# Optimization experiments

Measured on AMD Instinct MI355X. Metric: run time of the kernel, lower is better.

Reference implementation:

```python
import jax, jax.numpy as jnp
import numpy as np

B, L, F, R = 8, 64, 64, 2048

def setup_inputs() -> dict:
    key = jax.random.key(0)
    k1, k2, k3, k4, k5, k6, k7 = jax.random.split(key, 7)
    return {
        "x": jax.random.normal(k1, (B, L, F, R), dtype=jnp.float32),
        "arg1_weight": jax.random.uniform(k2, (B, L), dtype=jnp.float32),
        "arg2_weight": jax.random.uniform(k3, (B, L), dtype=jnp.float32),
        "root_filler": jax.random.normal(k4, (B, F), dtype=jnp.float32),
        "cons_l": jax.random.normal(k5, (R, R), dtype=jnp.float32) / np.sqrt(R).astype(np.float32),
        "cons_r": jax.random.normal(k6, (R, R), dtype=jnp.float32) / np.sqrt(R).astype(np.float32),
        "root_role": jax.random.normal(k7, (R,), dtype=jnp.float32),
    }

def reference(x, arg1_weight, arg2_weight, root_filler, cons_l, cons_r, root_role):
    # Weighted reduction over memory slots: [B,L,F,R] x [B,L] -> [B,F,R]
    arg1 = jnp.einsum('blfr,bl->bfr', x, arg1_weight)
    arg2 = jnp.einsum('blfr,bl->bfr', x, arg2_weight)
    # F.linear on last (role) dim: y = arg @ W^T, plus root outer product
    output = (jnp.einsum('bfr,sr->bfs', arg1, cons_l)
              + jnp.einsum('bfr,sr->bfs', arg2, cons_r)
              + root_filler[:, :, None] * root_role[None, None, :])
    max1 = jnp.max(arg1_weight, axis=1)
    max2 = jnp.max(arg2_weight, axis=1)
    return (output, max1, max2)
```

## Files before the change

kernel.cpp:

```cpp
#include <hip/hip_runtime.h>
#include <hip/hip_bf16.h>
#include <stdint.h>

#define B_DIM 8
#define L_DIM 64
#define F_DIM 64
#define R_DIM 2048
#define M_DIM 512
#define K_DIM 4096
#define N_DIM 2048

typedef _Float16 half_t;
typedef _Float16 half4 __attribute__((ext_vector_type(4)));
typedef _Float16 half8 __attribute__((ext_vector_type(8)));
typedef float floatx4 __attribute__((ext_vector_type(4)));
typedef float f4 __attribute__((ext_vector_type(4)));

__global__ __launch_bounds__(512) void k_front(
    const float* __restrict__ x, const float* __restrict__ w1,
    const float* __restrict__ w2, const float* __restrict__ cl,
    const float* __restrict__ cr, half_t* __restrict__ Ah,
    half_t* __restrict__ Bh, float* __restrict__ out)
{
    const int tid = threadIdx.x;
    const int bid = blockIdx.x;

    if (bid < 512) {
        __shared__ float w1s[L_DIM], w2s[L_DIM];
        const int bf = bid;
        const int b  = bf >> 6;
        const int f  = bf & 63;
        if (tid < L_DIM) {
            w1s[tid] = w1[b * L_DIM + tid];
            w2s[tid] = w2[b * L_DIM + tid];
        }
        __syncthreads();
        const int r0 = tid * 4;
        const f4* xp = (const f4*)(x + ((size_t)(b * 4096 + f)) * 2048 + r0);
        float a1x=0.f,a1y=0.f,a1z=0.f,a1w=0.f;
        float a2x=0.f,a2y=0.f,a2z=0.f,a2w=0.f;
        #pragma unroll 8
        for (int l = 0; l < L_DIM; ++l) {
            f4 v = __builtin_nontemporal_load(xp + (size_t)l * (F_DIM * R_DIM / 4));
            float u1 = w1s[l], u2 = w2s[l];
            a1x += v.x*u1; a1y += v.y*u1; a1z += v.z*u1; a1w += v.w*u1;
            a2x += v.x*u2; a2y += v.y*u2; a2z += v.z*u2; a2w += v.w*u2;
        }
        half4 h1 = { (half_t)a1x, (half_t)a1y, (half_t)a1z, (half_t)a1w };
        half4 h2 = { (half_t)a2x, (half_t)a2y, (half_t)a2z, (half_t)a2w };
        *(half4*)(Ah + (size_t)bf * K_DIM + r0) = h1;
        *(half4*)(Ah + (size_t)bf * K_DIM + R_DIM + r0) = h2;
    } else if (bid < 2560) {
        const int i = ((bid - 512) * 512 + tid) * 4;
        const int s = i >> 11;
        const int r = i & 2047;
        f4 vl = __builtin_nontemporal_load((const f4*)(cl + i));
        f4 vr = __builtin_nontemporal_load((const f4*)(cr + i));
        half4 hl = { (half_t)vl.x, (half_t)vl.y, (half_t)vl.z, (half_t)vl.w };
        half4 hr = { (half_t)vr.x, (half_t)vr.y, (half_t)vr.z, (half_t)vr.w };
        *(half4*)(Bh + (size_t)s * K_DIM + r) = hl;
        *(half4*)(Bh + (size_t)s * K_DIM + R_DIM + r) = hr;
    } else {
        if (tid < 16) {
            const float* src = (tid < 8) ? w1 : w2;
            const int b = tid & 7;
            float m = -1.f;
            #pragma unroll 8
            for (int l = 0; l < L_DIM; ++l)
                m = fmaxf(m, src[b * L_DIM + l]);
            out[M_DIM * N_DIM + tid] = m;
        }
    }
}

__device__ __forceinline__ void gload16(void* lds, const void* g)
{
    __builtin_amdgcn_global_load_lds(
        (const __attribute__((address_space(1))) void*)g,
        (__attribute__((address_space(3))) void*)lds, 16, 0, 0);
}

#define BM 128
#define BN 128
#define BK 64
#define SPLITK 8
#define KSEG (K_DIM / SPLITK)
#define NSTEP (KSEG / BK)

__global__ __launch_bounds__(256) void k_gemm(
    const half_t* __restrict__ Ah, const half_t* __restrict__ Bh,
    float* __restrict__ part)
{
    __shared__ half_t sA[2][BM * BK];
    __shared__ half_t sB[2][BN * BK];
    const int tid  = threadIdx.x;
    const int lane = tid & 63;
    const int w    = tid >> 6;
    const int wr   = w >> 1, wc = w & 1;
    const int m0   = blockIdx.y * BM;
    const int n0   = blockIdx.x * BN;
    const int kz   = blockIdx.z * KSEG;

    const int srow = lane >> 3;
    const int scol = ((lane & 7) ^ srow) << 3;

    const floatx4 fzero = { 0.f, 0.f, 0.f, 0.f };
    floatx4 acc[4][4];
    #pragma unroll
    for (int i = 0; i < 4; ++i)
        #pragma unroll
        for (int j = 0; j < 4; ++j) acc[i][j] = fzero;

    auto stage = [&](int buf, int kt) {
        #pragma unroll
        for (int c = 0; c < 4; ++c) {
            const int rbase = w * 32 + c * 8;
            const int row   = rbase + srow;
            gload16(&sA[buf][rbase * BK], Ah + (size_t)(m0 + row) * K_DIM + kt + scol);
            gload16(&sB[buf][rbase * BK], Bh + (size_t)(n0 + row) * K_DIM + kt + scol);
        }
    };

    stage(0, kz);
    __syncthreads();

    const int l15 = lane & 15, l4 = lane >> 4;
    int buf = 0;
    for (int ks = 0; ks < NSTEP; ++ks) {
        if (ks + 1 < NSTEP) stage(buf ^ 1, kz + (ks + 1) * BK);
        #pragma unroll
        for (int ksub = 0; ksub < 2; ++ksub) {
            half8 af[4], bfr[4];
            const int cb = ksub * 4 + l4;
            #pragma unroll
            for (int mi = 0; mi < 4; ++mi) {
                const int row = wr * 64 + mi * 16 + l15;
                af[mi] = *(const half8*)&sA[buf][row * BK + ((cb ^ (row & 7)) << 3)];
            }
            #pragma unroll
            for (int ni = 0; ni < 4; ++ni) {
                const int row = wc * 64 + ni * 16 + l15;
                bfr[ni] = *(const half8*)&sB[buf][row * BK + ((cb ^ (row & 7)) << 3)];
            }
            #pragma unroll
            for (int mi = 0; mi < 4; ++mi)
                #pragma unroll
                for (int ni = 0; ni < 4; ++ni)
                    acc[mi][ni] = __builtin_amdgcn_mfma_f32_16x16x32_f16(
                        af[mi], bfr[ni], acc[mi][ni], 0, 0, 0);
        }
        __syncthreads();
        buf ^= 1;
    }

    float* P = part + (size_t)blockIdx.z * ((size_t)M_DIM * N_DIM);
    #pragma unroll
    for (int mi = 0; mi < 4; ++mi) {
        const int rb = m0 + wr * 64 + mi * 16 + l4 * 4;
        #pragma unroll
        for (int ni = 0; ni < 4; ++ni) {
            const int cc = n0 + wc * 64 + ni * 16 + l15;
            #pragma unroll
            for (int r = 0; r < 4; ++r)
                P[(size_t)(rb + r) * N_DIM + cc] = acc[mi][ni][r];
        }
    }
}

__global__ __launch_bounds__(256) void k_final(
    const float* __restrict__ part, const float* __restrict__ filler,
    const float* __restrict__ role, float* __restrict__ out)
{
    const int idx = (blockIdx.x * 256 + threadIdx.x) * 4;
    const int mfi = idx >> 11;
    const int s   = idx & 2047;
    float4 a = *(const float4*)(part + idx);
    #pragma unroll
    for (int z = 1; z < SPLITK; ++z) {
        float4 p = *(const float4*)(part + (size_t)z * (M_DIM * N_DIM) + idx);
        a.x += p.x; a.y += p.y; a.z += p.z; a.w += p.w;
    }
    const float fl = filler[mfi];
    float4 ro = *(const float4*)(role + s);
    a.x += fl * ro.x; a.y += fl * ro.y; a.z += fl * ro.z; a.w += fl * ro.w;
    *(float4*)(out + idx) = a;
}

extern "C" void kernel_launch(void* const* d_in, const int* in_sizes, int n_in,
                              void* d_out, int out_size, void* d_ws, size_t ws_size,
                              hipStream_t stream)
{
    const float* x      = (const float*)d_in[0];
    const float* w1     = (const float*)d_in[1];
    const float* w2     = (const float*)d_in[2];
    const float* filler = (const float*)d_in[3];
    const float* cl     = (const float*)d_in[4];
    const float* cr     = (const float*)d_in[5];
    const float* role   = (const float*)d_in[6];
    float* out = (float*)d_out;

    char* ws = (char*)d_ws;
    half_t* Ah  = (half_t*)ws;
    half_t* Bh  = (half_t*)(ws + (4u << 20));
    float*  prt = (float*)(ws + (20u << 20));

    hipLaunchKernelGGL(k_front, dim3(2561), dim3(512), 0, stream,
                       x, w1, w2, cl, cr, Ah, Bh, out);
    hipLaunchKernelGGL(k_gemm,  dim3(N_DIM / BN, M_DIM / BM, SPLITK), dim3(256), 0, stream,
                       Ah, Bh, prt);
    hipLaunchKernelGGL(k_final, dim3(1024), dim3(256), 0, stream, prt, filler, role, out);
}
```

Before: 82.22 us.

## Fuse front, GEMM and reduction into one cooperative persistent kernel

Replaces the three launches (reduce/convert, split-K GEMM, final sum) with a single cooperative kernel of 256 blocks separated by grid-wide syncs. Split-K drops from 8 to 4 and the per-block GEMM tile becomes 128x128 across 8 waves, each computing 64x32. The aim is to remove launch gaps and shrink the partial-sum traffic. The cost is far fewer blocks and waves in the memory-bound front phase (256 blocks instead of 2561), plus grid-sync overhead.

Measured after the change: 298.3 us. +262.8%, slower.

```diff
diff --git a/kernel.cpp b/kernel.cpp
--- a/kernel.cpp
+++ b/kernel.cpp
@@ -1,77 +1,24 @@
 #include <hip/hip_runtime.h>
-#include <hip/hip_bf16.h>
+#include <hip/hip_cooperative_groups.h>
 #include <stdint.h>
 
-#define B_DIM 8
+namespace cg = cooperative_groups;
+
 #define L_DIM 64
-#define F_DIM 64
 #define R_DIM 2048
 #define M_DIM 512
 #define K_DIM 4096
 #define N_DIM 2048
+#define SPLITK 4
+#define KSEG (K_DIM / SPLITK)
+#define BK 64
+#define NSTEP (KSEG / BK)
 
 typedef _Float16 half_t;
 typedef _Float16 half4 __attribute__((ext_vector_type(4)));
 typedef _Float16 half8 __attribute__((ext_vector_type(8)));
+typedef float f4 __attribute__((ext_vector_type(4)));
 typedef float floatx4 __attribute__((ext_vector_type(4)));
-typedef float f4 __attribute__((ext_vector_type(4)));
-
-__global__ __launch_bounds__(512) void k_front(
-    const float* __restrict__ x, const float* __restrict__ w1,
-    const float* __restrict__ w2, const float* __restrict__ cl,
-    const float* __restrict__ cr, half_t* __restrict__ Ah,
-    half_t* __restrict__ Bh, float* __restrict__ out)
-{
-    const int tid = threadIdx.x;
-    const int bid = blockIdx.x;
-
-    if (bid < 512) {
-        __shared__ float w1s[L_DIM], w2s[L_DIM];
-        const int bf = bid;
-        const int b  = bf >> 6;
-        const int f  = bf & 63;
-        if (tid < L_DIM) {
-            w1s[tid] = w1[b * L_DIM + tid];
-            w2s[tid] = w2[b * L_DIM + tid];
-        }
-        __syncthreads();
-        const int r0 = tid * 4;
-        const f4* xp = (const f4*)(x + ((size_t)(b * 4096 + f)) * 2048 + r0);
-        float a1x=0.f,a1y=0.f,a1z=0.f,a1w=0.f;
-        float a2x=0.f,a2y=0.f,a2z=0.f,a2w=0.f;
-        #pragma unroll 8
-        for (int l = 0; l < L_DIM; ++l) {
-            f4 v = __builtin_nontemporal_load(xp + (size_t)l * (F_DIM * R_DIM / 4));
-            float u1 = w1s[l], u2 = w2s[l];
-            a1x += v.x*u1; a1y += v.y*u1; a1z += v.z*u1; a1w += v.w*u1;
-            a2x += v.x*u2; a2y += v.y*u2; a2z += v.z*u2; a2w += v.w*u2;
-        }
-        half4 h1 = { (half_t)a1x, (half_t)a1y, (half_t)a1z, (half_t)a1w };
-        half4 h2 = { (half_t)a2x, (half_t)a2y, (half_t)a2z, (half_t)a2w };
-        *(half4*)(Ah + (size_t)bf * K_DIM + r0) = h1;
-        *(half4*)(Ah + (size_t)bf * K_DIM + R_DIM + r0) = h2;
-    } else if (bid < 2560) {
-        const int i = ((bid - 512) * 512 + tid) * 4;
-        const int s = i >> 11;
-        const int r = i & 2047;
-        f4 vl = __builtin_nontemporal_load((const f4*)(cl + i));
-        f4 vr = __builtin_nontemporal_load((const f4*)(cr + i));
-        half4 hl = { (half_t)vl.x, (half_t)vl.y, (half_t)vl.z, (half_t)vl.w };
-        half4 hr = { (half_t)vr.x, (half_t)vr.y, (half_t)vr.z, (half_t)vr.w };
-        *(half4*)(Bh + (size_t)s * K_DIM + r) = hl;
-        *(half4*)(Bh + (size_t)s * K_DIM + R_DIM + r) = hr;
-    } else {
-        if (tid < 16) {
-            const float* src = (tid < 8) ? w1 : w2;
-            const int b = tid & 7;
-            float m = -1.f;
-            #pragma unroll 8
-            for (int l = 0; l < L_DIM; ++l)
-                m = fmaxf(m, src[b * L_DIM + l]);
-            out[M_DIM * N_DIM + tid] = m;
-        }
-    }
-}
 
 __device__ __forceinline__ void gload16(void* lds, const void* g)
 {
@@ -80,110 +27,178 @@
         (__attribute__((address_space(3))) void*)lds, 16, 0, 0);
 }
 
-#define BM 128
-#define BN 128
-#define BK 64
-#define SPLITK 8
-#define KSEG (K_DIM / SPLITK)
-#define NSTEP (KSEG / BK)
-
-__global__ __launch_bounds__(256) void k_gemm(
-    const half_t* __restrict__ Ah, const half_t* __restrict__ Bh,
-    float* __restrict__ part)
+__global__ __launch_bounds__(512, 2) void k_all(
+    const float* __restrict__ x, const float* __restrict__ w1,
+    const float* __restrict__ w2, const float* __restrict__ cl,
+    const float* __restrict__ cr, const float* __restrict__ filler,
+    const float* __restrict__ role, half_t* __restrict__ Ah,
+    half_t* __restrict__ Bh, float* __restrict__ part,
+    float* __restrict__ out)
 {
-    __shared__ half_t sA[2][BM * BK];
-    __shared__ half_t sB[2][BN * BK];
-    const int tid  = threadIdx.x;
-    const int lane = tid & 63;
-    const int w    = tid >> 6;
-    const int wr   = w >> 1, wc = w & 1;
-    const int m0   = blockIdx.y * BM;
-    const int n0   = blockIdx.x * BN;
-    const int kz   = blockIdx.z * KSEG;
-
-    const int srow = lane >> 3;
-    const int scol = ((lane & 7) ^ srow) << 3;
-
-    const floatx4 fzero = { 0.f, 0.f, 0.f, 0.f };
-    floatx4 acc[4][4];
+    __shared__ char smem[65536];
+    const int tid = threadIdx.x;
+    const int bid = blockIdx.x;
+    cg::grid_group grid = cg::this_grid();
+
+    {
+        float* w1s = (float*)smem;
+        float* w2s = w1s + L_DIM;
+        const int b = bid >> 5;
+        if (tid < L_DIM) {
+            w1s[tid] = w1[b * L_DIM + tid];
+            w2s[tid] = w2[b * L_DIM + tid];
+        }
+        __syncthreads();
+
+        #pragma unroll
+        for (int rr = 0; rr < 2; ++rr) {
+            const int bf = bid * 2 + rr;
+            const int f  = bf & 63;
+            const int r0 = tid * 4;
+            const f4* xp = (const f4*)(x + ((size_t)(b * 4096 + f)) * 2048 + r0);
+            float a1x=0.f,a1y=0.f,a1z=0.f,a1w=0.f;
+            float a2x=0.f,a2y=0.f,a2z=0.f,a2w=0.f;
+            #pragma unroll 8
+            for (int l = 0; l < L_DIM; ++l) {
+                f4 v = __builtin_nontemporal_load(xp + (size_t)l * (64 * R_DIM / 4));
+                float u1 = w1s[l], u2 = w2s[l];
+                a1x += v.x*u1; a1y += v.y*u1; a1z += v.z*u1; a1w += v.w*u1;
+                a2x += v.x*u2; a2y += v.y*u2; a2z += v.z*u2; a2w += v.w*u2;
+            }
+            half4 h1 = { (half_t)a1x, (half_t)a1y, (half_t)a1z, (half_t)a1w };
+            half4 h2 = { (half_t)a2x, (half_t)a2y, (half_t)a2z, (half_t)a2w };
+            *(half4*)(Ah + (size_t)bf * K_DIM + r0) = h1;
+            *(half4*)(Ah + (size_t)bf * K_DIM + R_DIM + r0) = h2;
+        }
+
+        #pragma unroll
+        for (int it = 0; it < 8; ++it) {
+            const int i = ((it * 131072) + bid * 512 + tid) * 4;
+            const int s = i >> 11;
+            const int r = i & 2047;
+            f4 vl = __builtin_nontemporal_load((const f4*)(cl + i));
+            f4 vr = __builtin_nontemporal_load((const f4*)(cr + i));
+            half4 hl = { (half_t)vl.x, (half_t)vl.y, (half_t)vl.z, (half_t)vl.w };
+            half4 hr = { (half_t)vr.x, (half_t)vr.y, (half_t)vr.z, (half_t)vr.w };
+            *(half4*)(Bh + (size_t)s * K_DIM + r) = hl;
+            *(half4*)(Bh + (size_t)s * K_DIM + R_DIM + r) = hr;
+        }
+
+        if (bid == 0 && tid < 16) {
+            const float* src = (tid < 8) ? w1 : w2;
+            const int b8 = tid & 7;
+            float m = -1.f;
+            #pragma unroll 8
+            for (int l = 0; l < L_DIM; ++l)
+                m = fmaxf(m, src[b8 * L_DIM + l]);
+            out[(size_t)M_DIM * N_DIM + tid] = m;
+        }
+    }
+
+    __threadfence();
+    grid.sync();
+
+    {
+        const int lane = tid & 63;
+        const int w    = tid >> 6;
+        const int wr   = w >> 2;
+        const int wc   = w & 3;
+        const int z    = bid >> 6;
+        const int mblk = (bid >> 4) & 3;
+        const int nblk = bid & 15;
+        const int m0   = mblk * 128;
+        const int n0   = nblk * 128;
+        const int kz   = z * KSEG;
+
+        const int srow = lane >> 3;
+        const int scol = ((lane & 7) ^ srow) << 3;
+
+        const floatx4 fzero = { 0.f, 0.f, 0.f, 0.f };
+        floatx4 acc[4][2];
+        #pragma unroll
+        for (int i = 0; i < 4; ++i)
+            #pragma unroll
+            for (int j = 0; j < 2; ++j) acc[i][j] = fzero;
+
+        auto stage = [&](int buf, int kt) {
+            half_t* sA = (half_t*)smem + buf * 8192;
+            half_t* sB = (half_t*)(smem + 32768) + buf * 8192;
+            #pragma unroll
+            for (int c = 0; c < 2; ++c) {
+                const int rbase = w * 16 + c * 8;
+                const int row   = rbase + srow;
+                gload16(&sA[rbase * 64], Ah + (size_t)(m0 + row) * K_DIM + kt + scol);
+                gload16(&sB[rbase * 64], Bh + (size_t)(n0 + row) * K_DIM + kt + scol);
+            }
+        };
+
+        stage(0, kz);
+        __syncthreads();
+
+        const int l15 = lane & 15, l4 = lane >> 4;
+        int buf = 0;
+        for (int ks = 0; ks < NSTEP; ++ks) {
+            if (ks + 1 < NSTEP) stage(buf ^ 1, kz + (ks + 1) * BK);
+            half_t* sA = (half_t*)smem + buf * 8192;
+            half_t* sB = (half_t*)(smem + 32768) + buf * 8192;
+            #pragma unroll
+            for (int ksub = 0; ksub < 2; ++ksub) {
+                half8 af[4], bf2[2];
+                const int cb = ksub * 4 + l4;
+                #pragma unroll
+                for (int mi = 0; mi < 4; ++mi) {
+                    const int row = wr * 64 + mi * 16 + l15;
+                    af[mi] = *(const half8*)&sA[row * 64 + ((cb ^ (row & 7)) << 3)];
+                }
+                #pragma unroll
+                for (int ni = 0; ni < 2; ++ni) {
+                    const int row = wc * 32 + ni * 16 + l15;
+                    bf2[ni] = *(const half8*)&sB[row * 64 + ((cb ^ (row & 7)) << 3)];
+                }
+                #pragma unroll
+                for (int mi = 0; mi < 4; ++mi)
+                    #pragma unroll
+                    for (int ni = 0; ni < 2; ++ni)
+                        acc[mi][ni] = __builtin_amdgcn_mfma_f32_16x16x32_f16(
+                            af[mi], bf2[ni], acc[mi][ni], 0, 0, 0);
+            }
+            __syncthreads();
+            buf ^= 1;
+        }
+
+        float* P = part + (size_t)z * ((size_t)M_DIM * N_DIM);
+        #pragma unroll
+        for (int mi = 0; mi < 4; ++mi) {
+            const int rb = m0 + wr * 64 + mi * 16 + l4 * 4;
+            #pragma unroll
+            for (int ni = 0; ni < 2; ++ni) {
+                const int cc = n0 + wc * 32 + ni * 16 + l15;
+                #pragma unroll
+                for (int r = 0; r < 4; ++r)
+                    P[(size_t)(rb + r) * N_DIM + cc] = acc[mi][ni][r];
+            }
+        }
+    }
+
+    __threadfence();
+    grid.sync();
+
     #pragma unroll
-    for (int i = 0; i < 4; ++i)
-        #pragma unroll
-        for (int j = 0; j < 4; ++j) acc[i][j] = fzero;
-
-    auto stage = [&](int buf, int kt) {
-        #pragma unroll
-        for (int c = 0; c < 4; ++c) {
-            const int rbase = w * 32 + c * 8;
-            const int row   = rbase + srow;
-            gload16(&sA[buf][rbase * BK], Ah + (size_t)(m0 + row) * K_DIM + kt + scol);
-            gload16(&sB[buf][rbase * BK], Bh + (size_t)(n0 + row) * K_DIM + kt + scol);
-        }
-    };
-
-    stage(0, kz);
-    __syncthreads();
-
-    const int l15 = lane & 15, l4 = lane >> 4;
-    int buf = 0;
-    for (int ks = 0; ks < NSTEP; ++ks) {
-        if (ks + 1 < NSTEP) stage(buf ^ 1, kz + (ks + 1) * BK);
-        #pragma unroll
-        for (int ksub = 0; ksub < 2; ++ksub) {
-            half8 af[4], bfr[4];
-            const int cb = ksub * 4 + l4;
-            #pragma unroll
-            for (int mi = 0; mi < 4; ++mi) {
-                const int row = wr * 64 + mi * 16 + l15;
-                af[mi] = *(const half8*)&sA[buf][row * BK + ((cb ^ (row & 7)) << 3)];
-            }
-            #pragma unroll
-            for (int ni = 0; ni < 4; ++ni) {
-                const int row = wc * 64 + ni * 16 + l15;
-                bfr[ni] = *(const half8*)&sB[buf][row * BK + ((cb ^ (row & 7)) << 3)];
-            }
-            #pragma unroll
-            for (int mi = 0; mi < 4; ++mi)
-                #pragma unroll
-                for (int ni = 0; ni < 4; ++ni)
-                    acc[mi][ni] = __builtin_amdgcn_mfma_f32_16x16x32_f16(
-                        af[mi], bfr[ni], acc[mi][ni], 0, 0, 0);
-        }
-        __syncthreads();
-        buf ^= 1;
+    for (int it = 0; it < 2; ++it) {
+        const int idx = ((it * 131072) + bid * 512 + tid) * 4;
+        const int mfi = idx >> 11;
+        const int s   = idx & 2047;
+        f4 a = *(const f4*)(part + idx);
+        #pragma unroll
+        for (int z = 1; z < SPLITK; ++z) {
+            f4 p = *(const f4*)(part + (size_t)z * (M_DIM * (size_t)N_DIM) + idx);
+            a.x += p.x; a.y += p.y; a.z += p.z; a.w += p.w;
+        }
+        const float fl = filler[mfi];
+        f4 ro = *(const f4*)(role + s);
+        a.x += fl * ro.x; a.y += fl * ro.y; a.z += fl * ro.z; a.w += fl * ro.w;
+        *(f4*)(out + idx) = a;
     }
-
-    float* P = part + (size_t)blockIdx.z * ((size_t)M_DIM * N_DIM);
-    #pragma unroll
-    for (int mi = 0; mi < 4; ++mi) {
-        const int rb = m0 + wr * 64 + mi * 16 + l4 * 4;
-        #pragma unroll
-        for (int ni = 0; ni < 4; ++ni) {
-            const int cc = n0 + wc * 64 + ni * 16 + l15;
-            #pragma unroll
-            for (int r = 0; r < 4; ++r)
-                P[(size_t)(rb + r) * N_DIM + cc] = acc[mi][ni][r];
-        }
-    }
-}
-
-__global__ __launch_bounds__(256) void k_final(
-    const float* __restrict__ part, const float* __restrict__ filler,
-    const float* __restrict__ role, float* __restrict__ out)
-{
-    const int idx = (blockIdx.x * 256 + threadIdx.x) * 4;
-    const int mfi = idx >> 11;
-    const int s   = idx & 2047;
-    float4 a = *(const float4*)(part + idx);
-    #pragma unroll
-    for (int z = 1; z < SPLITK; ++z) {
-        float4 p = *(const float4*)(part + (size_t)z * (M_DIM * N_DIM) + idx);
-        a.x += p.x; a.y += p.y; a.z += p.z; a.w += p.w;
-    }
-    const float fl = filler[mfi];
-    float4 ro = *(const float4*)(role + s);
-    a.x += fl * ro.x; a.y += fl * ro.y; a.z += fl * ro.z; a.w += fl * ro.w;
-    *(float4*)(out + idx) = a;
 }
 
 extern "C" void kernel_launch(void* const* d_in, const int* in_sizes, int n_in,
@@ -204,9 +219,9 @@
     half_t* Bh  = (half_t*)(ws + (4u << 20));
     float*  prt = (float*)(ws + (20u << 20));
 
-    hipLaunchKernelGGL(k_front, dim3(2561), dim3(512), 0, stream,
-                       x, w1, w2, cl, cr, Ah, Bh, out);
-    hipLaunchKernelGGL(k_gemm,  dim3(N_DIM / BN, M_DIM / BM, SPLITK), dim3(256), 0, stream,
-                       Ah, Bh, prt);
-    hipLaunchKernelGGL(k_final, dim3(1024), dim3(256), 0, stream, prt, filler, role, out);
+    void* args[] = { (void*)&x, (void*)&w1, (void*)&w2, (void*)&cl, (void*)&cr,
+                     (void*)&filler, (void*)&role, (void*)&Ah, (void*)&Bh,
+                     (void*)&prt, (void*)&out };
+    hipLaunchCooperativeKernel((const void*)k_all, dim3(256), dim3(512),
+                               args, 0, stream);
 }
```

## Replace split-K partial buffer and final reduce with atomic accumulation into output

Applied to the files above, without the earlier changes.

The front kernel now also writes the root outer-product term into the output, and its weight-conversion work is folded into the 512 reduction blocks instead of separate blocks. The GEMM then atomically adds its split-K partial results directly into the output, so the final reduction kernel and the 8-way partial buffer traffic are removed. In exchange, the GEMM epilogue issues many scalar float atomics, which may contend and make the summation order nondeterministic.

Result: slower. 96.55 us (+17.4%).

```diff
diff --git a/kernel.cpp b/kernel.cpp
--- a/kernel.cpp
+++ b/kernel.cpp
@@ -1,10 +1,7 @@
 #include <hip/hip_runtime.h>
-#include <hip/hip_bf16.h>
 #include <stdint.h>
 
-#define B_DIM 8
 #define L_DIM 64
-#define F_DIM 64
 #define R_DIM 2048
 #define M_DIM 512
 #define K_DIM 4096
@@ -13,35 +10,36 @@
 typedef _Float16 half_t;
 typedef _Float16 half4 __attribute__((ext_vector_type(4)));
 typedef _Float16 half8 __attribute__((ext_vector_type(8)));
+typedef float f4 __attribute__((ext_vector_type(4)));
 typedef float floatx4 __attribute__((ext_vector_type(4)));
-typedef float f4 __attribute__((ext_vector_type(4)));
 
 __global__ __launch_bounds__(512) void k_front(
     const float* __restrict__ x, const float* __restrict__ w1,
     const float* __restrict__ w2, const float* __restrict__ cl,
-    const float* __restrict__ cr, half_t* __restrict__ Ah,
+    const float* __restrict__ cr, const float* __restrict__ filler,
+    const float* __restrict__ role, half_t* __restrict__ Ah,
     half_t* __restrict__ Bh, float* __restrict__ out)
 {
     const int tid = threadIdx.x;
-    const int bid = blockIdx.x;
-
-    if (bid < 512) {
-        __shared__ float w1s[L_DIM], w2s[L_DIM];
-        const int bf = bid;
-        const int b  = bf >> 6;
-        const int f  = bf & 63;
-        if (tid < L_DIM) {
-            w1s[tid] = w1[b * L_DIM + tid];
-            w2s[tid] = w2[b * L_DIM + tid];
-        }
-        __syncthreads();
+    const int bf  = blockIdx.x;
+    const int b   = bf >> 6;
+    const int f   = bf & 63;
+
+    __shared__ float w1s[L_DIM], w2s[L_DIM];
+    if (tid < L_DIM) {
+        w1s[tid] = w1[b * L_DIM + tid];
+        w2s[tid] = w2[b * L_DIM + tid];
+    }
+    __syncthreads();
+
+    {
         const int r0 = tid * 4;
         const f4* xp = (const f4*)(x + ((size_t)(b * 4096 + f)) * 2048 + r0);
         float a1x=0.f,a1y=0.f,a1z=0.f,a1w=0.f;
         float a2x=0.f,a2y=0.f,a2z=0.f,a2w=0.f;
         #pragma unroll 8
         for (int l = 0; l < L_DIM; ++l) {
-            f4 v = __builtin_nontemporal_load(xp + (size_t)l * (F_DIM * R_DIM / 4));
+            f4 v = __builtin_nontemporal_load(xp + (size_t)l * (64 * R_DIM / 4));
             float u1 = w1s[l], u2 = w2s[l];
             a1x += v.x*u1; a1y += v.y*u1; a1z += v.z*u1; a1w += v.w*u1;
             a2x += v.x*u2; a2y += v.y*u2; a2z += v.z*u2; a2w += v.w*u2;
@@ -50,8 +48,11 @@
         half4 h2 = { (half_t)a2x, (half_t)a2y, (half_t)a2z, (half_t)a2w };
         *(half4*)(Ah + (size_t)bf * K_DIM + r0) = h1;
         *(half4*)(Ah + (size_t)bf * K_DIM + R_DIM + r0) = h2;
-    } else if (bid < 2560) {
-        const int i = ((bid - 512) * 512 + tid) * 4;
+    }
+
+    #pragma unroll
+    for (int it = 0; it < 4; ++it) {
+        const int i = (((bf * 4 + it) * 512) + tid) * 4;
         const int s = i >> 11;
         const int r = i & 2047;
         f4 vl = __builtin_nontemporal_load((const f4*)(cl + i));
@@ -60,16 +61,26 @@
         half4 hr = { (half_t)vr.x, (half_t)vr.y, (half_t)vr.z, (half_t)vr.w };
         *(half4*)(Bh + (size_t)s * K_DIM + r) = hl;
         *(half4*)(Bh + (size_t)s * K_DIM + R_DIM + r) = hr;
-    } else {
-        if (tid < 16) {
-            const float* src = (tid < 8) ? w1 : w2;
-            const int b = tid & 7;
-            float m = -1.f;
-            #pragma unroll 8
-            for (int l = 0; l < L_DIM; ++l)
-                m = fmaxf(m, src[b * L_DIM + l]);
-            out[M_DIM * N_DIM + tid] = m;
-        }
+    }
+
+    {
+        const int j   = (bf * 512 + tid) * 4;
+        const int mfi = j >> 11;
+        const int s   = j & 2047;
+        const float fl = filler[mfi];
+        f4 ro = *(const f4*)(role + s);
+        f4 o = { fl * ro.x, fl * ro.y, fl * ro.z, fl * ro.w };
+        *(f4*)(out + j) = o;
+    }
+
+    if (bf == 0 && tid < 16) {
+        const float* src = (tid < 8) ? w1 : w2;
+        const int b8 = tid & 7;
+        float m = -1.f;
+        #pragma unroll 8
+        for (int l = 0; l < L_DIM; ++l)
+            m = fmaxf(m, src[b8 * L_DIM + l]);
+        out[(size_t)M_DIM * N_DIM + tid] = m;
     }
 }
 
@@ -89,7 +100,7 @@
 
 __global__ __launch_bounds__(256) void k_gemm(
     const half_t* __restrict__ Ah, const half_t* __restrict__ Bh,
-    float* __restrict__ part)
+    float* __restrict__ out)
 {
     __shared__ half_t sA[2][BM * BK];
     __shared__ half_t sB[2][BN * BK];
@@ -153,7 +164,6 @@
         buf ^= 1;
     }
 
-    float* P = part + (size_t)blockIdx.z * ((size_t)M_DIM * N_DIM);
     #pragma unroll
     for (int mi = 0; mi < 4; ++mi) {
         const int rb = m0 + wr * 64 + mi * 16 + l4 * 4;
@@ -162,28 +172,9 @@
             const int cc = n0 + wc * 64 + ni * 16 + l15;
             #pragma unroll
             for (int r = 0; r < 4; ++r)
-                P[(size_t)(rb + r) * N_DIM + cc] = acc[mi][ni][r];
-        }
-    }
-}
-
-__global__ __launch_bounds__(256) void k_final(
-    const float* __restrict__ part, const float* __restrict__ filler,
-    const float* __restrict__ role, float* __restrict__ out)
-{
-    const int idx = (blockIdx.x * 256 + threadIdx.x) * 4;
-    const int mfi = idx >> 11;
-    const int s   = idx & 2047;
-    float4 a = *(const float4*)(part + idx);
-    #pragma unroll
-    for (int z = 1; z < SPLITK; ++z) {
-        float4 p = *(const float4*)(part + (size_t)z * (M_DIM * N_DIM) + idx);
-        a.x += p.x; a.y += p.y; a.z += p.z; a.w += p.w;
-    }
-    const float fl = filler[mfi];
-    float4 ro = *(const float4*)(role + s);
-    a.x += fl * ro.x; a.y += fl * ro.y; a.z += fl * ro.z; a.w += fl * ro.w;
-    *(float4*)(out + idx) = a;
+                atomicAdd(&out[(size_t)(rb + r) * N_DIM + cc], acc[mi][ni][r]);
+        }
+    }
 }
 
 extern "C" void kernel_launch(void* const* d_in, const int* in_sizes, int n_in,
@@ -202,11 +193,9 @@
     char* ws = (char*)d_ws;
     half_t* Ah  = (half_t*)ws;
     half_t* Bh  = (half_t*)(ws + (4u << 20));
-    float*  prt = (float*)(ws + (20u << 20));
-
-    hipLaunchKernelGGL(k_front, dim3(2561), dim3(512), 0, stream,
-                       x, w1, w2, cl, cr, Ah, Bh, out);
+
+    hipLaunchKernelGGL(k_front, dim3(512), dim3(512), 0, stream,
+                       x, w1, w2, cl, cr, filler, role, Ah, Bh, out);
     hipLaunchKernelGGL(k_gemm,  dim3(N_DIM / BN, M_DIM / BM, SPLITK), dim3(256), 0, stream,
-                       Ah, Bh, prt);
-    hipLaunchKernelGGL(k_final, dim3(1024), dim3(256), 0, stream, prt, filler, role, out);
-}
+                       Ah, Bh, out);
+}
```
